# Performance work log

Hardware: AMD Instinct MI355X
Metric: run time of the kernel (lower is better)

## Reference

```python
import jax, jax.numpy as jnp
import numpy as np

D_MODEL = 1024
N_HEADS = 16
K_TOP = 64
D_HEAD = D_MODEL // N_HEADS


def setup_inputs() -> dict:
    key = jax.random.key(0)
    ks = jax.random.split(key, 9)
    B, L = 8, 4096
    bound = 1.0 / np.sqrt(D_MODEL)  # nn.Linear default init range
    lin = lambda k: jax.random.uniform(k, (D_MODEL, D_MODEL), jnp.float32, -bound, bound)
    vec = lambda k: jax.random.uniform(k, (D_MODEL,), jnp.float32, -bound, bound)
    return {
        "query": jax.random.normal(ks[0], (B, L, D_MODEL), jnp.float32),
        "Wq": lin(ks[1]), "bq": vec(ks[2]),
        "Wk": lin(ks[3]), "bk": vec(ks[4]),
        "Wv": lin(ks[5]), "bv": vec(ks[6]),
        "Wo": lin(ks[7]), "bo": vec(ks[8]),
    }


def reference(query, Wq, bq, Wk, bk, Wv, bv, Wo, bo):
    B, L_q, D = query.shape
    L_k = L_q  # self-attention: key = value = query
    F_q = L_q // 2 + 1
    F_k = L_k // 2 + 1
    k_top = min(K_TOP, F_q)

    def proj(x, W, b):
        # (B, L, D) -> (B, H, L, d_head)
        return (x @ W + b).reshape(B, -1, N_HEADS, D_HEAD).transpose(0, 2, 1, 3)

    q = proj(query, Wq, bq)
    k = proj(query, Wk, bk)
    v = proj(query, Wv, bv)

    q_freq = jnp.fft.rfft(q, axis=2)  # (B, H, F_q, d_head) complex64
    k_freq = jnp.fft.rfft(k, axis=2)
    v_freq = jnp.fft.rfft(v, axis=2)

    # top-k frequency bins by mean spectral magnitude of the query
    q_energy = jnp.abs(q_freq).mean(axis=-1)  # (B, H, F_q)
    _, idx = jax.lax.top_k(q_energy, k_top)   # (B, H, k)
    mapped_idx = jnp.clip(
        jnp.round(idx.astype(jnp.float32) * (F_k - 1) / (F_q - 1)).astype(jnp.int32),
        0, F_k - 1)

    gather = lambda x, i: jnp.take_along_axis(x, i[..., None], axis=2)
    q_top = gather(q_freq, idx)          # (B, H, k, d_head)
    k_top_freq = gather(k_freq, mapped_idx)
    v_top = gather(v_freq, mapped_idx)

    eps = 1e-8
    attn_score = (q_top.real * k_top_freq.real).sum(-1) / (D_HEAD ** 0.5 + eps)
    attn = jax.nn.softmax(attn_score, axis=-1)[..., None]  # (B, H, k, 1)

    # fill spectrum with mean of query spectrum, then scatter attended bins
    q_mean_freq = q_freq.mean(axis=2, keepdims=True)  # (B, H, 1, d_head) complex
    out_freq = jnp.broadcast_to(q_mean_freq, (B, N_HEADS, F_q, D_HEAD))
    src = (attn * v_top.real).astype(out_freq.dtype)  # real -> complex (imag=0)
    bi = jnp.arange(B)[:, None, None]
    hi = jnp.arange(N_HEADS)[None, :, None]
    out_freq = out_freq.at[bi, hi, idx].set(src)

    out_time = jnp.fft.irfft(out_freq, n=L_q, axis=2)  # (B, H, L, d_head)
    out = out_time.transpose(0, 2, 1, 3).reshape(B, L_q, D)
    return out @ Wo + bo
```

## Files before the change

kernel.cpp:

```cpp
#include <hip/hip_runtime.h>
#include <math.h>
#include <stdint.h>


typedef _Float16 f16;
typedef _Float16 f16x8 __attribute__((ext_vector_type(8)));
typedef float f32x4 __attribute__((ext_vector_type(4)));

#define PI_F 3.14159265358979323846f
#define PADJ(j) ((j) + ((j) >> 3))

__device__ __forceinline__ void gl_lds16(const void* g, void* l) {
  __builtin_amdgcn_global_load_lds((const __attribute__((address_space(1))) void*)g,
                                   (__attribute__((address_space(3))) void*)l, 16, 0, 0);
}

__device__ __forceinline__ float2 cadd(float2 a, float2 b) { return make_float2(a.x + b.x, a.y + b.y); }
__device__ __forceinline__ float2 csub(float2 a, float2 b) { return make_float2(a.x - b.x, a.y - b.y); }
__device__ __forceinline__ float2 cmul(float2 a, float2 b) {
  return make_float2(a.x * b.x - a.y * b.y, a.x * b.y + a.y * b.x);
}
__device__ __forceinline__ float2 cmni(float2 a) { return make_float2(a.y, -a.x); }

template <int NIT>
__device__ __forceinline__ void stgP(const char* g, size_t gstride, int kb, char* lds,
                                     int tid, int w) {
#pragma unroll
  for (int it = 0; it < NIT; ++it) {
    int ls = it * 256 + tid;
    int j = ls >> 3, s = ls & 7;
    int u = s ^ (j & 7);
    int grow = 2 * j + (u >> 2);
    gl_lds16(g + (size_t)grow * gstride + ((u & 3) << 4) + kb, lds + it * 4096 + w * 1024);
  }
}

__device__ __forceinline__ int pofs(int grow, int q) {
  int j = grow >> 1;
  int u = ((grow & 1) << 2) | q;
  return j * 128 + ((u ^ (j & 7)) << 4);
}

__global__ __launch_bounds__(256) void k_tw(float2* __restrict__ twtab, float2* __restrict__ utab) {
  int j = blockIdx.x * 256 + threadIdx.x;
  if (j < 2048) {
    float ang = (float)j * (-6.28318530717958647692f / 2048.0f);
    twtab[j] = make_float2(cosf(ang), sinf(ang));
  } else if (j < 4097) {
    int f = j - 2048;
    float ang = (float)f * (-6.28318530717958647692f / 4096.0f);
    utab[f] = make_float2(cosf(ang), sinf(ang));
  }
}

__global__ __launch_bounds__(256) void k_prep(const float* __restrict__ Wq, const float* __restrict__ Wo,
                                              f16* __restrict__ WqT, f16* __restrict__ WoT) {
  __shared__ float t[32][33];
  const float* src = blockIdx.z ? Wo : Wq;
  f16* dst = blockIdx.z ? WoT : WqT;
  int c0 = blockIdx.x * 32, r0 = blockIdx.y * 32;
  int tx = threadIdx.x, ty = threadIdx.y;
#pragma unroll
  for (int yy = 0; yy < 4; ++yy)
    t[ty + yy * 8][tx] = src[(size_t)(r0 + ty + yy * 8) * 1024 + c0 + tx];
  __syncthreads();
#pragma unroll
  for (int yy = 0; yy < 4; ++yy)
    dst[(size_t)(c0 + ty + yy * 8) * 1024 + r0 + tx] = (f16)t[tx][ty + yy * 8];
}

__global__ __launch_bounds__(256) void k_prep2(const float* __restrict__ Wk, const float* __restrict__ Wv,
                                               f16* __restrict__ WkT, f16* __restrict__ WvT) {
  __shared__ float t[32][33];
  const float* src = blockIdx.z ? Wv : Wk;
  f16* dst = blockIdx.z ? WvT : WkT;
  int c0 = blockIdx.x * 32, r0 = blockIdx.y * 32;
  int tx = threadIdx.x, ty = threadIdx.y;
#pragma unroll
  for (int yy = 0; yy < 4; ++yy)
    t[ty + yy * 8][tx] = src[(size_t)(r0 + ty + yy * 8) * 1024 + c0 + tx];
  __syncthreads();
#pragma unroll
  for (int yy = 0; yy < 4; ++yy)
    dst[(size_t)(c0 + ty + yy * 8) * 1024 + r0 + tx] = (f16)t[tx][ty + yy * 8];
}

__global__ __launch_bounds__(256) void k_t1(const float* __restrict__ X, float* __restrict__ Xt) {
  __shared__ float t[32][33];
  int b = blockIdx.z;
  int l0 = blockIdx.x * 32, d0 = blockIdx.y * 32;
  int tx = threadIdx.x, ty = threadIdx.y;
#pragma unroll
  for (int yy = 0; yy < 4; ++yy)
    t[ty + yy * 8][tx] = X[((size_t)b * 4096 + l0 + ty + yy * 8) * 1024 + d0 + tx];
  __syncthreads();
#pragma unroll
  for (int yy = 0; yy < 4; ++yy)
    Xt[((size_t)b * 1024 + d0 + ty + yy * 8) * 4096 + l0 + tx] = t[tx][ty + yy * 8];
}

__device__ __forceinline__ void r8_stage(const float2* __restrict__ cur, float2* __restrict__ nxt,
                                         const float2* __restrict__ tw, int tid, int lg) {
  int Ls = 1 << lg;
  int p = tid >> lg, q = tid & (Ls - 1);
  float2 x[8];
#pragma unroll
  for (int u = 0; u < 8; ++u) x[u] = cur[PADJ(tid + 256 * u)];
  float2 s0 = cadd(x[0], x[4]), d0v = csub(x[0], x[4]);
  float2 s1 = cadd(x[2], x[6]), d1v = csub(x[2], x[6]);
  float2 e0 = cadd(s0, s1), e2 = csub(s0, s1);
  float2 md1 = cmni(d1v);
  float2 e1 = cadd(d0v, md1), e3 = csub(d0v, md1);
  float2 t0 = cadd(x[1], x[5]), u0 = csub(x[1], x[5]);
  float2 t1 = cadd(x[3], x[7]), u1 = csub(x[3], x[7]);
  float2 o0 = cadd(t0, t1), o2 = csub(t0, t1);
  float2 mu1 = cmni(u1);
  float2 o1 = cadd(u0, mu1), o3 = csub(u0, mu1);
  const float C8 = 0.70710678118654752440f;
  float2 w1 = make_float2(C8 * (o1.x + o1.y), C8 * (o1.y - o1.x));
  float2 w2 = cmni(o2);
  float2 w3 = make_float2(C8 * (o3.y - o3.x), -C8 * (o3.x + o3.y));
  float2 y[8];
  y[0] = cadd(e0, o0); y[4] = csub(e0, o0);
  y[1] = cadd(e1, w1); y[5] = csub(e1, w1);
  y[2] = cadd(e2, w2); y[6] = csub(e2, w2);
  y[3] = cadd(e3, w3); y[7] = csub(e3, w3);
  int tb = p << lg;
#pragma unroll
  for (int v = 1; v < 8; ++v) y[v] = cmul(y[v], tw[tb * v]);
  int ob = q + (p << (lg + 3));
#pragma unroll
  for (int v = 0; v < 8; ++v) nxt[PADJ(ob + (v << lg))] = y[v];
}

__global__ __launch_bounds__(256) void k_fft(const float* __restrict__ Xt,
                                             const float2* __restrict__ twtab,
                                             const float2* __restrict__ utab,
                                             f16* __restrict__ PReU, f16* __restrict__ PImU,
                                             float* __restrict__ sumXf) {
  __shared__ float2 bufA[2304];
  __shared__ float2 bufB[2304];
  __shared__ float redr[256], redi[256];
  int tid = threadIdx.x;
  int blk = blockIdx.x;

  const float4* src = (const float4*)(Xt + (size_t)blk * 4096);
#pragma unroll
  for (int r = 0; r < 4; ++r) {
    int i4 = r * 256 + tid;
    float4 v = src[i4];
    bufA[PADJ(2 * i4)] = make_float2(v.x, v.y);
    bufA[PADJ(2 * i4 + 1)] = make_float2(v.z, v.w);
  }
  __syncthreads();
  r8_stage(bufA, bufB, twtab, tid, 0);
  __syncthreads();
  r8_stage(bufB, bufA, twtab, tid, 3);
  __syncthreads();
  r8_stage(bufA, bufB, twtab, tid, 6);
  __syncthreads();
#pragma unroll
  for (int h = 0; h < 2; ++h) {
    int i = (h << 8) + tid;
    float2 a0 = bufB[PADJ(i)], a1 = bufB[PADJ(i + 512)];
    float2 a2 = bufB[PADJ(i + 1024)], a3 = bufB[PADJ(i + 1536)];
    float2 s02 = cadd(a0, a2), d02 = csub(a0, a2);
    float2 s13 = cadd(a1, a3), d13m = cmni(csub(a1, a3));
    bufA[PADJ(i)] = cadd(s02, s13);
    bufA[PADJ(i + 512)] = cadd(d02, d13m);
    bufA[PADJ(i + 1024)] = csub(s02, s13);
    bufA[PADJ(i + 1536)] = csub(d02, d13m);
  }
  __syncthreads();
  float sumr = 0.f, sumi = 0.f;
  size_t obase = (size_t)blk * 2049;
  for (int f = tid; f <= 2048; f += 256) {
    int fz = f & 2047, fm = (2048 - f) & 2047;
    float2 z = bufA[PADJ(fz)], m = bufA[PADJ(fm)];
    float Er = 0.5f * (z.x + m.x), Ei = 0.5f * (z.y - m.y);
    float Or = 0.5f * (z.y + m.y), Oi = -0.5f * (z.x - m.x);
    float2 wv = utab[f];
    float Xr = Er + wv.x * Or - wv.y * Oi;
    float Xi = Ei + wv.x * Oi + wv.y * Or;
    PReU[obase + f] = (f16)Xr;
    PImU[obase + f] = (f16)Xi;
    sumr += Xr; sumi += Xi;
  }
  __syncthreads();
  redr[tid] = sumr; redi[tid] = sumi;
  __syncthreads();
  for (int s = 128; s > 0; s >>= 1) {
    if (tid < s) { redr[tid] += redr[tid + s]; redi[tid] += redi[tid + s]; }
    __syncthreads();
  }
  if (tid == 0) { sumXf[2 * blk] = redr[0]; sumXf[2 * blk + 1] = redi[0]; }
}

__global__ __launch_bounds__(256) void k_C(const float* __restrict__ sumXf, const float* __restrict__ Wq,
                                           const float* __restrict__ bq,
                                           float* __restrict__ Cre, float* __restrict__ Cim) {
  int b = blockIdx.x >> 2;
  int hd = ((blockIdx.x & 3) << 8) + threadIdx.x;
  float accr = 0.f, acci = 0.f;
  for (int dm = 0; dm < 1024; ++dm) {
    float w = Wq[(size_t)dm * 1024 + hd];
    accr += sumXf[2 * (b * 1024 + dm)] * w;
    acci += sumXf[2 * (b * 1024 + dm) + 1] * w;
  }
  Cre[b * 1024 + hd] = (accr + 4096.0f * bq[hd]) * (1.0f / 2049.0f);
  Cim[b * 1024 + hd] = acci * (1.0f / 2049.0f);
}

__global__ __launch_bounds__(256) void k_t2(const f16* __restrict__ PReU, const f16* __restrict__ PImU,
                                            f16* __restrict__ PT) {
  __shared__ f16 t[32][33];
  int z = blockIdx.z;
  int b = z >> 1, pl = z & 1;
  const f16* src = pl ? PImU : PReU;
  int f0 = blockIdx.x * 32, d0 = blockIdx.y * 32;
  int tx = threadIdx.x, ty = threadIdx.y;
#pragma unroll
  for (int yy = 0; yy < 4; ++yy) {
    int ff = f0 + tx;
    t[ty + yy * 8][tx] = (ff < 2049) ? src[(size_t)(b * 1024 + d0 + ty + yy * 8) * 2049 + ff] : (f16)0.f;
  }
  __syncthreads();
#pragma unroll
  for (int yy = 0; yy < 4; ++yy)
    PT[((size_t)b * 4352 + 2 * (f0 + ty + yy * 8) + pl) * 1024 + d0 + tx] = t[tx][ty + yy * 8];
}

__global__ __launch_bounds__(256, 2) void k_energy(const f16* __restrict__ PT, const f16* __restrict__ WqT,
                                                   const float* __restrict__ bq, float* __restrict__ energy) {
  __shared__ __align__(16) char sM[2][24576];
  int tid = threadIdx.x;
  int lane = tid & 63, w = tid >> 6;
  int lin = blockIdx.x;
  int sw = (lin & 7) * 136 + (lin >> 3);
  int bN = sw & 3, Mblk = sw >> 2;
  int wr = w >> 1, wc = w & 1;
  f32x4 acc[4][8];
#pragma unroll
  for (int mf = 0; mf < 4; ++mf)
#pragma unroll
    for (int nf = 0; nf < 8; ++nf) acc[mf][nf] = 0;

  const char* gA0 = (const char*)PT + (size_t)(Mblk * 128) * 2048;
  const char* gB0 = (const char*)WqT + (size_t)(bN * 256) * 2048;
  int r = lane & 15, q = lane >> 4;
  int aofs[4], bofs[8];
#pragma unroll
  for (int mf = 0; mf < 4; ++mf) aofs[mf] = pofs(wr * 64 + mf * 16 + r, q);
#pragma unroll
  for (int nf = 0; nf < 8; ++nf) bofs[nf] = 8192 + pofs(wc * 128 + nf * 16 + r, q);

  char* b0 = &sM[0][0];
  char* b1 = &sM[1][0];
  auto compute = [&](const char* base) {
    f16x8 aF[4], bF[8];
#pragma unroll
    for (int mf = 0; mf < 4; ++mf) aF[mf] = *(const f16x8*)(base + aofs[mf]);
#pragma unroll
    for (int nf = 0; nf < 8; ++nf) bF[nf] = *(const f16x8*)(base + bofs[nf]);
#pragma unroll
    for (int mf = 0; mf < 4; ++mf)
#pragma unroll
      for (int nf = 0; nf < 8; ++nf)
        acc[mf][nf] = __builtin_amdgcn_mfma_f32_16x16x32_f16(aF[mf], bF[nf], acc[mf][nf], 0, 0, 0);
  };

  stgP<2>(gA0, 2048, 0, b0, tid, w);
  stgP<4>(gB0, 2048, 0, b0 + 8192, tid, w);
  for (int t = 0; t < 16; ++t) {
    int kb1 = (2 * t + 1) * 64;
    stgP<2>(gA0, 2048, kb1, b1, tid, w);
    stgP<4>(gB0, 2048, kb1, b1 + 8192, tid, w);
    asm volatile("s_waitcnt vmcnt(6)\ns_barrier" ::: "memory");
    compute(b0);
    asm volatile("s_barrier" ::: "memory");
    if (t < 15) {
      int kb0 = (2 * t + 2) * 64;
      stgP<2>(gA0, 2048, kb0, b0, tid, w);
      stgP<4>(gB0, 2048, kb0, b0 + 8192, tid, w);
      asm volatile("s_waitcnt vmcnt(6)\ns_barrier" ::: "memory");
    } else {
      asm volatile("s_waitcnt vmcnt(0)\ns_barrier" ::: "memory");
    }
    compute(b1);
    asm volatile("s_barrier" ::: "memory");
  }
  int b = Mblk / 34;
  int tIb = Mblk - b * 34;
  int h0 = bN * 4 + wc * 2;
  bool dc0 = (tIb == 0 && wr == 0 && q == 0);
#pragma unroll
  for (int mf = 0; mf < 4; ++mf) {
    float sE0 = 0.f, sO0 = 0.f, sE1 = 0.f, sO1 = 0.f;
#pragma unroll
    for (int nf = 0; nf < 8; ++nf) {
      float re0 = acc[mf][nf][0], im0 = acc[mf][nf][1];
      float re1 = acc[mf][nf][2], im1 = acc[mf][nf][3];
      if (dc0 && mf == 0) re0 += 4096.0f * bq[(h0 + (nf >> 2)) * 64 + (nf & 3) * 16 + r];
      float m0 = sqrtf(re0 * re0 + im0 * im0);
      float m1 = sqrtf(re1 * re1 + im1 * im1);
      if (nf < 4) { sE0 += m0; sO0 += m1; } else { sE1 += m0; sO1 += m1; }
    }
#pragma unroll
    for (int off = 1; off < 16; off <<= 1) {
      sE0 += __shfl_xor(sE0, off);
      sO0 += __shfl_xor(sO0, off);
      sE1 += __shfl_xor(sE1, off);
      sO1 += __shfl_xor(sO1, off);
    }
    if (r == 0) {
      int fp = tIb * 64 + wr * 32 + mf * 8 + (q << 1);
      energy[((size_t)b * 16 + h0) * 2176 + fp] = sE0 * 0.015625f;
      energy[((size_t)b * 16 + h0) * 2176 + fp + 1] = sO0 * 0.015625f;
      energy[((size_t)b * 16 + h0 + 1) * 2176 + fp] = sE1 * 0.015625f;
      energy[((size_t)b * 16 + h0 + 1) * 2176 + fp + 1] = sO1 * 0.015625f;
    }
  }
}

__global__ __launch_bounds__(256) void k_topk(const float* __restrict__ energy, int* __restrict__ idxb) {
  __shared__ float vals[2049];
  __shared__ unsigned long long wbest[4];
  int tid = threadIdx.x, bh = blockIdx.x;
  const float* e = energy + (size_t)bh * 2176;
  for (int i = tid; i < 2049; i += 256) vals[i] = e[i];
  __syncthreads();
  for (int it = 0; it < 64; ++it) {
    unsigned long long best = 0ull;
    for (int f = tid; f < 2049; f += 256) {
      unsigned b32 = __float_as_uint(vals[f]);
      b32 = (b32 & 0x80000000u) ? ~b32 : (b32 | 0x80000000u);
      unsigned long long k = ((unsigned long long)b32 << 12) | (unsigned)(4095 - f);
      best = (k > best) ? k : best;
    }
#pragma unroll
    for (int off = 32; off > 0; off >>= 1) {
      unsigned long long o = __shfl_xor(best, off);
      best = (o > best) ? o : best;
    }
    if ((tid & 63) == 0) wbest[tid >> 6] = best;
    __syncthreads();
    if (tid == 0) {
      unsigned long long b0 = wbest[0] > wbest[1] ? wbest[0] : wbest[1];
      unsigned long long b1 = wbest[2] > wbest[3] ? wbest[2] : wbest[3];
      unsigned long long bb = b0 > b1 ? b0 : b1;
      int f = 4095 - (int)(bb & 4095ull);
      idxb[bh * 64 + it] = f;
      vals[f] = -1.0f;
    }
    __syncthreads();
  }
}

__global__ __launch_bounds__(256) void k_qkv(const f16* __restrict__ PT, const int* __restrict__ idxb,
                                             const f16* __restrict__ WqT, const f16* __restrict__ WkT,
                                             const f16* __restrict__ WvT, float* __restrict__ part) {
  __shared__ __align__(16) f16 sA[64 * 64];
  __shared__ __align__(16) f16 sB[192 * 64];
  __shared__ int fjs[64];
  int tid = threadIdx.x, lane = tid & 63, w = tid >> 6;
  int bh = blockIdx.x, ks = blockIdx.y;
  int b = bh >> 4, h = bh & 15;
  if (tid < 64) fjs[tid] = idxb[bh * 64 + tid];
  __syncthreads();
  f32x4 acc[4][3];
#pragma unroll
  for (int mf = 0; mf < 4; ++mf)
#pragma unroll
    for (int nf = 0; nf < 3; ++nf) acc[mf][nf] = 0;

  int l8 = lane & 7;
  int lr = lane >> 3;
  int swz = (l8 ^ lr) << 4;

  for (int kt = 0; kt < 4; ++kt) {
    int kbyte = ks * 512 + kt * 128;
#pragma unroll
    for (int t = 0; t < 2; ++t) {
      int ia = w * 2 + t;
      int row = ia * 8 + lr;
      const char* src = (const char*)PT + (size_t)(b * 4352 + 2 * fjs[row]) * 2048 + kbyte + swz;
      gl_lds16(src, (char*)sA + ia * 1024);
    }
#pragma unroll
    for (int t = 0; t < 6; ++t) {
      int ib = w * 6 + t;
      int row = ib * 8 + lr;
      const f16* Wt = (row < 64) ? WqT : (row < 128) ? WkT : WvT;
      const char* src = (const char*)Wt + (size_t)(h * 64 + (row & 63)) * 2048 + kbyte + swz;
      gl_lds16(src, (char*)sB + ib * 1024);
    }
    __syncthreads();
#pragma unroll
    for (int kk = 0; kk < 64; kk += 32) {
      int cb = (kk << 1) + ((lane >> 4) << 4);
      int r = lane & 15;
      f16x8 aF[4], bF[3];
#pragma unroll
      for (int mf = 0; mf < 4; ++mf) {
        int row = mf * 16 + r;
        aF[mf] = *(const f16x8*)((const char*)sA + row * 128 + (cb ^ ((row & 7) << 4)));
      }
#pragma unroll
      for (int nf = 0; nf < 3; ++nf) {
        int row = w * 48 + nf * 16 + r;
        bF[nf] = *(const f16x8*)((const char*)sB + row * 128 + (cb ^ ((row & 7) << 4)));
      }
#pragma unroll
      for (int mf = 0; mf < 4; ++mf)
#pragma unroll
        for (int nf = 0; nf < 3; ++nf)
          acc[mf][nf] = __builtin_amdgcn_mfma_f32_16x16x32_f16(aF[mf], bF[nf], acc[mf][nf], 0, 0, 0);
    }
    __syncthreads();
  }
  float* pb = part + (size_t)(ks * 128 + bh) * 12288;
#pragma unroll
  for (int mf = 0; mf < 4; ++mf)
#pragma unroll
    for (int nf = 0; nf < 3; ++nf)
#pragma unroll
      for (int rr = 0; rr < 4; ++rr) {
        int m = mf * 16 + ((lane >> 4) << 2) + rr;
        int n = w * 48 + nf * 16 + (lane & 15);
        pb[m * 192 + n] = acc[mf][nf][rr];
      }
}

__global__ __launch_bounds__(256) void k_attn2(const float* __restrict__ part, const int* __restrict__ idxb,
                                               const float* __restrict__ bq, const float* __restrict__ bk,
                                               const float* __restrict__ bv, const float* __restrict__ Cre,
                                               f16* __restrict__ ampT) {
  __shared__ float sQKV[64][196];
  __shared__ float scores[64], attns[64];
  __shared__ int fjs[64];
  __shared__ int dcrow;
  int tid = threadIdx.x, bh = blockIdx.x;
  int b = bh >> 4, h = bh & 15;
  if (tid == 0) dcrow = -1;
  __syncthreads();
  if (tid < 64) {
    int f = idxb[bh * 64 + tid];
    fjs[tid] = f;
    if (f == 0) dcrow = tid;
  }
  __syncthreads();
  const float4* p0 = (const float4*)(part + (size_t)bh * 12288);
  const size_t s4 = (size_t)128 * 12288 / 4;
#pragma unroll
  for (int it = 0; it < 12; ++it) {
    int e = it * 256 + tid;
    float4 v0 = p0[e], v1 = p0[e + s4], v2 = p0[e + 2 * s4], v3 = p0[e + 3 * s4];
    float4 v;
    v.x = v0.x + v1.x + v2.x + v3.x;
    v.y = v0.y + v1.y + v2.y + v3.y;
    v.z = v0.z + v1.z + v2.z + v3.z;
    v.w = v0.w + v1.w + v2.w + v3.w;
    int m = e / 48, n0 = (e % 48) * 4;
    *(float4*)&sQKV[m][n0] = v;
  }
  __syncthreads();
  if (dcrow >= 0 && tid < 192) {
    const float* bias = (tid < 64) ? bq : (tid < 128) ? bk : bv;
    sQKV[dcrow][tid] += 4096.0f * bias[h * 64 + (tid & 63)];
  }
  __syncthreads();
  {
    int j = tid >> 2, p = tid & 3;
    float s = 0.f;
#pragma unroll
    for (int c = 0; c < 16; ++c) {
      int cc = p * 16 + c;
      s = fmaf(sQKV[j][cc], sQKV[j][64 + cc], s);
    }
    s += __shfl_xor(s, 1);
    s += __shfl_xor(s, 2);
    if (p == 0) scores[j] = s * 0.125f;
  }
  __syncthreads();
  if (tid < 64) {
    float s = scores[tid];
    float m = s;
#pragma unroll
    for (int off = 32; off > 0; off >>= 1) m = fmaxf(m, __shfl_xor(m, off));
    float ev = expf(s - m);
    float sm = ev;
#pragma unroll
    for (int off = 32; off > 0; off >>= 1) sm += __shfl_xor(sm, off);
    attns[tid] = ev / sm;
  }
  __syncthreads();
  {
    int j = tid >> 2, d0 = (tid & 3) * 16;
    float at = attns[j];
    int fj = fjs[j];
    float wj = (fj == 0 || fj == 2048) ? 0.5f : 1.0f;
#pragma unroll
    for (int q4 = 0; q4 < 4; ++q4) {
      float4 c4 = *(const float4*)&Cre[b * 1024 + h * 64 + d0 + q4 * 4];
      float4 vv = *(const float4*)&sQKV[j][128 + d0 + q4 * 4];
      float av0 = wj * (at * vv.x - c4.x);
      float av1 = wj * (at * vv.y - c4.y);
      float av2 = wj * (at * vv.z - c4.z);
      float av3 = wj * (at * vv.w - c4.w);
      f16* o = ampT + (size_t)bh * 4096 + (d0 + q4 * 4) * 64 + j;
      o[0] = (f16)av0; o[64] = (f16)av1; o[128] = (f16)av2; o[192] = (f16)av3;
    }
  }
}

__global__ __launch_bounds__(256) void k_ot(const f16* __restrict__ ampT, const int* __restrict__ idxb,
                                            const float* __restrict__ Cre, const float* __restrict__ Cim,
                                            f16* __restrict__ OT) {
  __shared__ __align__(16) f16 sAmp[64][72];
  __shared__ float gbuf[256];
  __shared__ int fjs[64];
  int tid = threadIdx.x, lane = tid & 63, w = tid >> 6;
  int bh = blockIdx.x >> 4, tch = blockIdx.x & 15;
  int b = bh >> 4, h = bh & 15;
  if (tid < 64) fjs[tid] = idxb[bh * 64 + tid];
  {
    int row = tid >> 2, seg = tid & 3;
    const f16* src = ampT + (size_t)bh * 4096 + row * 64 + seg * 16;
    f16x8 v0 = *(const f16x8*)src;
    f16x8 v1 = *(const f16x8*)(src + 8);
    *(f16x8*)&sAmp[row][seg * 16] = v0;
    *(f16x8*)&sAmp[row][seg * 16 + 8] = v1;
  }
  __syncthreads();
  int r = lane & 15, q = lane >> 4;
  int tbase = tch * 256 + w * 64;
  const float cang = 0.00153398078788564123f;
  f16x8 aF[4][2];
  float ss[4];
#pragma unroll
  for (int mf = 0; mf < 4; ++mf) {
    int t = tbase + mf * 16 + r;
    float s = 0.f;
#pragma unroll
    for (int kk2 = 0; kk2 < 2; ++kk2) {
      f16x8 a;
#pragma unroll
      for (int jj = 0; jj < 8; ++jj) {
        int j = kk2 * 32 + q * 8 + jj;
        int ridx = (fjs[j] * t) & 4095;
        float sn, cs;
        __sincosf((float)ridx * cang, &sn, &cs);
        s += sn;
        a[jj] = (f16)cs;
      }
      aF[mf][kk2] = a;
    }
    ss[mf] = s;
  }
#pragma unroll
  for (int mf = 0; mf < 4; ++mf) {
    ss[mf] += __shfl_xor(ss[mf], 16);
    ss[mf] += __shfl_xor(ss[mf], 32);
  }
  if (q == 0) {
#pragma unroll
    for (int mf = 0; mf < 4; ++mf) {
      int t = tbase + mf * 16 + r;
      float g = ss[mf];
      if (t & 1) {
        int tp = (t <= 2048) ? t : 4096 - t;
        float sg = (t <= 2048) ? 1.f : -1.f;
        float aa = (float)tp * (PI_F / 4096.0f);
        g -= sg * (cosf(aa) / sinf(aa));
      }
      gbuf[w * 64 + mf * 16 + r] = g;
    }
  }
  f16x8 bF[4][2];
#pragma unroll
  for (int nf = 0; nf < 4; ++nf)
#pragma unroll
    for (int kk2 = 0; kk2 < 2; ++kk2)
      bF[nf][kk2] = *(const f16x8*)&sAmp[nf * 16 + r][kk2 * 32 + q * 8];
  f32x4 acc[4][4];
#pragma unroll
  for (int mf = 0; mf < 4; ++mf)
#pragma unroll
    for (int nf = 0; nf < 4; ++nf) acc[mf][nf] = 0;
#pragma unroll
  for (int kk2 = 0; kk2 < 2; ++kk2)
#pragma unroll
    for (int mf = 0; mf < 4; ++mf)
#pragma unroll
      for (int nf = 0; nf < 4; ++nf)
        acc[mf][nf] = __builtin_amdgcn_mfma_f32_16x16x32_f16(aF[mf][kk2], bF[nf][kk2], acc[mf][nf], 0, 0, 0);
  __syncthreads();
  const float s2L = 2.0f / 4096.0f;
#pragma unroll
  for (int nf = 0; nf < 4; ++nf) {
    int d = nf * 16 + r;
    float cim = Cim[b * 1024 + h * 64 + d];
    float cre = Cre[b * 1024 + h * 64 + d];
#pragma unroll
    for (int mf = 0; mf < 4; ++mf) {
#pragma unroll
      for (int rr = 0; rr < 4; ++rr) {
        int ro = mf * 16 + q * 4 + rr;
        int t = tbase + ro;
        float g = gbuf[w * 64 + ro];
        float val = s2L * (acc[mf][nf][rr] + cim * g) + ((t == 0) ? cre : 0.f);
        OT[((size_t)bh * 4096 + t) * 64 + d] = (f16)val;
      }
    }
  }
}

__global__ __launch_bounds__(256, 2) void k_final(const f16* __restrict__ OT, const f16* __restrict__ WoT,
                                                  const float* __restrict__ bo, float* __restrict__ out) {
  __shared__ __align__(16) char sM[2][24576];
  int tid = threadIdx.x, lane = tid & 63, w = tid >> 6;
  int lin = blockIdx.x;
  int sw = (lin & 7) * 128 + (lin >> 3);
  int bN = sw & 3, Mblk = sw >> 2;
  int wr = w >> 1, wc = w & 1;
  f32x4 acc[4][8];
#pragma unroll
  for (int mf = 0; mf < 4; ++mf)
#pragma unroll
    for (int nf = 0; nf < 8; ++nf) acc[mf][nf] = 0;
  int b = Mblk >> 5, t0 = (Mblk & 31) * 128;
  const char* gB0 = (const char*)WoT + (size_t)(bN * 256) * 2048;
  int r = lane & 15, q = lane >> 4;
  int aofs[4], bofs[8];
#pragma unroll
  for (int mf = 0; mf < 4; ++mf) aofs[mf] = pofs(wr * 64 + mf * 16 + r, q);
#pragma unroll
  for (int nf = 0; nf < 8; ++nf) bofs[nf] = 8192 + pofs(wc * 128 + nf * 16 + r, q);
#define GA_HEAD(ks) ((const char*)OT + ((size_t)(b * 16 + ((ks) >> 1)) * 4096 + t0) * 128)

  char* b0 = &sM[0][0];
  char* b1 = &sM[1][0];
  auto compute = [&](const char* base) {
    f16x8 aF[4], bF[8];
#pragma unroll
    for (int mf = 0; mf < 4; ++mf) aF[mf] = *(const f16x8*)(base + aofs[mf]);
#pragma unroll
    for (int nf = 0; nf < 8; ++nf) bF[nf] = *(const f16x8*)(base + bofs[nf]);
#pragma unroll
    for (int mf = 0; mf < 4; ++mf)
#pragma unroll
      for (int nf = 0; nf < 8; ++nf)
        acc[mf][nf] = __builtin_amdgcn_mfma_f32_16x16x32_f16(aF[mf], bF[nf], acc[mf][nf], 0, 0, 0);
  };

  stgP<2>(GA_HEAD(0), 128, 0, b0, tid, w);
  stgP<4>(gB0, 2048, 0, b0 + 8192, tid, w);
  for (int t = 0; t < 16; ++t) {
    int ks1 = 2 * t + 1;
    stgP<2>(GA_HEAD(ks1), 128, (ks1 & 1) * 64, b1, tid, w);
    stgP<4>(gB0, 2048, ks1 * 64, b1 + 8192, tid, w);
    asm volatile("s_waitcnt vmcnt(6)\ns_barrier" ::: "memory");
    compute(b0);
    asm volatile("s_barrier" ::: "memory");
    if (t < 15) {
      int ks0 = 2 * t + 2;
      stgP<2>(GA_HEAD(ks0), 128, (ks0 & 1) * 64, b0, tid, w);
      stgP<4>(gB0, 2048, ks0 * 64, b0 + 8192, tid, w);
      asm volatile("s_waitcnt vmcnt(6)\ns_barrier" ::: "memory");
    } else {
      asm volatile("s_waitcnt vmcnt(0)\ns_barrier" ::: "memory");
    }
    compute(b1);
    asm volatile("s_barrier" ::: "memory");
  }
#undef GA_HEAD
#pragma unroll
  for (int nf = 0; nf < 8; ++nf) {
    int gcol = bN * 256 + wc * 128 + nf * 16 + r;
    float bcol = bo[gcol];
#pragma unroll
    for (int mf = 0; mf < 4; ++mf) {
#pragma unroll
      for (int rr = 0; rr < 4; ++rr) {
        int grow = Mblk * 128 + wr * 64 + mf * 16 + (q << 2) + rr;
        out[(size_t)grow * 1024 + gcol] = acc[mf][nf][rr] + bcol;
      }
    }
  }
}

extern "C" void kernel_launch(void* const* d_in, const int* in_sizes, int n_in,
                              void* d_out, int out_size, void* d_ws, size_t ws_size,
                              hipStream_t stream) {
  const float* X = (const float*)d_in[0];
  const float* Wq = (const float*)d_in[1];
  const float* bq = (const float*)d_in[2];
  const float* Wk = (const float*)d_in[3];
  const float* bk = (const float*)d_in[4];
  const float* Wv = (const float*)d_in[5];
  const float* bv = (const float*)d_in[6];
  const float* Wo = (const float*)d_in[7];
  const float* bo = (const float*)d_in[8];
  float* out = (float*)d_out;

  if (ws_size < 208928768ULL) return;
  char* w = (char*)d_ws;
  float* Xt = (float*)(w);
  f16* PT = (f16*)(w);
  f16* WkT = (f16*)(w + 71303168);
  f16* WvT = (f16*)(w + 73400320);
  float* part = (float*)(w + 75497472);
  char* R2 = w + 134217728;
  f16* PReU = (f16*)(R2);
  f16* PImU = (f16*)(R2 + 33570816);
  f16* OT = (f16*)(R2);
  char* R3 = R2 + 67141632;
  float* sumXf = (float*)(R3);
  float* Cre = (float*)(R3 + 65536);
  float* Cim = (float*)(R3 + 98304);
  float* energy = (float*)(R3 + 131072);
  int* idxb = (int*)(R3 + 1245184);
  f16* ampT = (f16*)(R3 + 1277952);
  f16* WqT = (f16*)(R3 + 3375104);
  f16* WoT = (f16*)(R3 + 5472256);
  float2* twtab = (float2*)d_out;
  float2* utab = twtab + 2048;

  dim3 b32(32, 8);
  hipLaunchKernelGGL(k_tw, dim3(17), dim3(256), 0, stream, twtab, utab);
  hipLaunchKernelGGL(k_prep, dim3(32, 32, 2), b32, 0, stream, Wq, Wo, WqT, WoT);
  hipLaunchKernelGGL(k_t1, dim3(128, 32, 8), b32, 0, stream, X, Xt);
  hipLaunchKernelGGL(k_fft, dim3(8192), dim3(256), 0, stream, Xt, twtab, utab, PReU, PImU, sumXf);
  hipLaunchKernelGGL(k_prep2, dim3(32, 32, 2), b32, 0, stream, Wk, Wv, WkT, WvT);
  hipLaunchKernelGGL(k_C, dim3(32), dim3(256), 0, stream, sumXf, Wq, bq, Cre, Cim);
  hipLaunchKernelGGL(k_t2, dim3(68, 32, 16), b32, 0, stream, PReU, PImU, PT);
  hipLaunchKernelGGL(k_energy, dim3(1088), dim3(256), 0, stream, PT, WqT, bq, energy);
  hipLaunchKernelGGL(k_topk, dim3(128), dim3(256), 0, stream, energy, idxb);
  hipLaunchKernelGGL(k_qkv, dim3(128, 4), dim3(256), 0, stream, PT, idxb, WqT, WkT, WvT, part);
  hipLaunchKernelGGL(k_attn2, dim3(128), dim3(256), 0, stream, part, idxb, bq, bk, bv, Cre, ampT);
  hipLaunchKernelGGL(k_ot, dim3(2048), dim3(256), 0, stream, ampT, idxb, Cre, Cim, OT);
  hipLaunchKernelGGL(k_final, dim3(1024), dim3(256), 0, stream, OT, WoT, bo, out);
}
```

Baseline: 509.9 us.

## Store transposed input as fp16 and raise MFMA wave priority

The transpose kernel now writes the time-major copy of the input in fp16 instead of fp32, using 64x64 tiles and vectorized 4-wide stores. The FFT kernel reads this half-precision buffer with 16-byte loads, which halves the intermediate write and read traffic. It also adds s_setprio around the MFMA loops in two GEMM kernels to favour matrix issue. Rounding the input to fp16 before the FFT adds precision loss.

Result: faster. 480.5 us (-5.8%).

```diff
diff --git a/kernel.cpp b/kernel.cpp
--- a/kernel.cpp
+++ b/kernel.cpp
@@ -4,6 +4,7 @@
 
 
 typedef _Float16 f16;
+typedef _Float16 f16x4 __attribute__((ext_vector_type(4)));
 typedef _Float16 f16x8 __attribute__((ext_vector_type(8)));
 typedef float f32x4 __attribute__((ext_vector_type(4)));
 
@@ -85,18 +86,26 @@
     dst[(size_t)(c0 + ty + yy * 8) * 1024 + r0 + tx] = (f16)t[tx][ty + yy * 8];
 }
 
-__global__ __launch_bounds__(256) void k_t1(const float* __restrict__ X, float* __restrict__ Xt) {
-  __shared__ float t[32][33];
+__global__ __launch_bounds__(256) void k_t1(const float* __restrict__ X, f16* __restrict__ Xt16) {
+  __shared__ float t[64][65];
   int b = blockIdx.z;
-  int l0 = blockIdx.x * 32, d0 = blockIdx.y * 32;
-  int tx = threadIdx.x, ty = threadIdx.y;
-#pragma unroll
-  for (int yy = 0; yy < 4; ++yy)
-    t[ty + yy * 8][tx] = X[((size_t)b * 4096 + l0 + ty + yy * 8) * 1024 + d0 + tx];
-  __syncthreads();
-#pragma unroll
-  for (int yy = 0; yy < 4; ++yy)
-    Xt[((size_t)b * 1024 + d0 + ty + yy * 8) * 4096 + l0 + tx] = t[tx][ty + yy * 8];
+  int l0 = blockIdx.x * 64, d0 = blockIdx.y * 64;
+  int tid = threadIdx.x;
+#pragma unroll
+  for (int it = 0; it < 16; ++it) {
+    int lr = it * 4 + (tid >> 6);
+    t[lr][tid & 63] = X[((size_t)b * 4096 + l0 + lr) * 1024 + d0 + (tid & 63)];
+  }
+  __syncthreads();
+#pragma unroll
+  for (int it = 0; it < 4; ++it) {
+    int dd = it * 16 + (tid >> 4);
+    int lc = (tid & 15) * 4;
+    f16x4 v;
+    v[0] = (f16)t[lc][dd]; v[1] = (f16)t[lc + 1][dd];
+    v[2] = (f16)t[lc + 2][dd]; v[3] = (f16)t[lc + 3][dd];
+    *(f16x4*)&Xt16[((size_t)b * 1024 + d0 + dd) * 4096 + l0 + lc] = v;
+  }
 }
 
 __device__ __forceinline__ void r8_stage(const float2* __restrict__ cur, float2* __restrict__ nxt,
@@ -133,7 +142,7 @@
   for (int v = 0; v < 8; ++v) nxt[PADJ(ob + (v << lg))] = y[v];
 }
 
-__global__ __launch_bounds__(256) void k_fft(const float* __restrict__ Xt,
+__global__ __launch_bounds__(256) void k_fft(const f16* __restrict__ Xt16,
                                              const float2* __restrict__ twtab,
                                              const float2* __restrict__ utab,
                                              f16* __restrict__ PReU, f16* __restrict__ PImU,
@@ -144,13 +153,14 @@
   int tid = threadIdx.x;
   int blk = blockIdx.x;
 
-  const float4* src = (const float4*)(Xt + (size_t)blk * 4096);
-#pragma unroll
-  for (int r = 0; r < 4; ++r) {
-    int i4 = r * 256 + tid;
-    float4 v = src[i4];
-    bufA[PADJ(2 * i4)] = make_float2(v.x, v.y);
-    bufA[PADJ(2 * i4 + 1)] = make_float2(v.z, v.w);
+  const f16x8* src = (const f16x8*)(Xt16 + (size_t)blk * 4096);
+#pragma unroll
+  for (int r = 0; r < 2; ++r) {
+    int i8 = r * 256 + tid;
+    f16x8 v = src[i8];
+#pragma unroll
+    for (int j = 0; j < 4; ++j)
+      bufA[PADJ(4 * i8 + j)] = make_float2((float)v[2 * j], (float)v[2 * j + 1]);
   }
   __syncthreads();
   r8_stage(bufA, bufB, twtab, tid, 0);
@@ -262,11 +272,13 @@
     for (int mf = 0; mf < 4; ++mf) aF[mf] = *(const f16x8*)(base + aofs[mf]);
 #pragma unroll
     for (int nf = 0; nf < 8; ++nf) bF[nf] = *(const f16x8*)(base + bofs[nf]);
+    __builtin_amdgcn_s_setprio(1);
 #pragma unroll
     for (int mf = 0; mf < 4; ++mf)
 #pragma unroll
       for (int nf = 0; nf < 8; ++nf)
         acc[mf][nf] = __builtin_amdgcn_mfma_f32_16x16x32_f16(aF[mf], bF[nf], acc[mf][nf], 0, 0, 0);
+    __builtin_amdgcn_s_setprio(0);
   };
 
   stgP<2>(gA0, 2048, 0, b0, tid, w);
@@ -646,11 +658,13 @@
     for (int mf = 0; mf < 4; ++mf) aF[mf] = *(const f16x8*)(base + aofs[mf]);
 #pragma unroll
     for (int nf = 0; nf < 8; ++nf) bF[nf] = *(const f16x8*)(base + bofs[nf]);
+    __builtin_amdgcn_s_setprio(1);
 #pragma unroll
     for (int mf = 0; mf < 4; ++mf)
 #pragma unroll
       for (int nf = 0; nf < 8; ++nf)
         acc[mf][nf] = __builtin_amdgcn_mfma_f32_16x16x32_f16(aF[mf], bF[nf], acc[mf][nf], 0, 0, 0);
+    __builtin_amdgcn_s_setprio(0);
   };
 
   stgP<2>(GA_HEAD(0), 128, 0, b0, tid, w);
@@ -705,7 +719,7 @@
 
   if (ws_size < 208928768ULL) return;
   char* w = (char*)d_ws;
-  float* Xt = (float*)(w);
+  f16* Xt16 = (f16*)(w);
   f16* PT = (f16*)(w);
   f16* WkT = (f16*)(w + 71303168);
   f16* WvT = (f16*)(w + 73400320);
@@ -729,8 +743,8 @@
   dim3 b32(32, 8);
   hipLaunchKernelGGL(k_tw, dim3(17), dim3(256), 0, stream, twtab, utab);
   hipLaunchKernelGGL(k_prep, dim3(32, 32, 2), b32, 0, stream, Wq, Wo, WqT, WoT);
-  hipLaunchKernelGGL(k_t1, dim3(128, 32, 8), b32, 0, stream, X, Xt);
-  hipLaunchKernelGGL(k_fft, dim3(8192), dim3(256), 0, stream, Xt, twtab, utab, PReU, PImU, sumXf);
+  hipLaunchKernelGGL(k_t1, dim3(64, 16, 8), dim3(256), 0, stream, X, Xt16);
+  hipLaunchKernelGGL(k_fft, dim3(8192), dim3(256), 0, stream, Xt16, twtab, utab, PReU, PImU, sumXf);
   hipLaunchKernelGGL(k_prep2, dim3(32, 32, 2), b32, 0, stream, Wk, Wv, WkT, WvT);
   hipLaunchKernelGGL(k_C, dim3(32), dim3(256), 0, stream, sumXf, Wq, bq, Cre, Cim);
   hipLaunchKernelGGL(k_t2, dim3(68, 32, 16), b32, 0, stream, PReU, PImU, PT);
```
